# Kernel optimization log

Measured on AMD Instinct MI355X. Metric: run time of the kernel, lower is better.

Reference implementation:

```python
import jax, jax.numpy as jnp
import numpy as np

TOPK = 2
RENORMALIZE = True

T, H, I, E = 2048, 2048, 5632, 8  # tokens, hidden, intermediate, experts


def setup_inputs() -> dict:
    key = jax.random.key(0)
    k1, k2, k3, k4 = jax.random.split(key, 4)
    x = jax.random.normal(k1, (T, H), dtype=jnp.float32)
    gating_output = jax.random.normal(k2, (T, E), dtype=jnp.float32)
    # gate_up_proj: concat of gate [E,I,H] and up [E,I,H] along dim 1 -> [E,2I,H]
    w1 = jax.random.normal(k3, (E, 2 * I, H), dtype=jnp.float32) * 0.02
    # down_proj: [E, H, I]
    w2 = jax.random.normal(k4, (E, H, I), dtype=jnp.float32) * 0.02
    return {"x": x, "gating_output": gating_output, "w1": w1, "w2": w2}


def _route(gating_output):
    # standard (non-grouped) top-k softmax routing, renormalized
    probs = jax.nn.softmax(gating_output, axis=-1)            # [T, E]
    topk_w, topk_idx = jax.lax.top_k(probs, TOPK)             # [T, K]
    if RENORMALIZE:
        topk_w = topk_w / jnp.sum(topk_w, axis=-1, keepdims=True)
    t = gating_output.shape[0]
    route = jnp.zeros((t, gating_output.shape[1]), dtype=topk_w.dtype)
    route = route.at[jnp.arange(t)[:, None], topk_idx].set(topk_w)  # [T, E]
    return route


def reference(x, gating_output, w1, w2):
    route = _route(gating_output)                             # [T, E]
    inter = w2.shape[-1]
    out = jnp.zeros_like(x)
    # loop over small fixed expert count; each iter is dense GEMM work
    for e in range(w1.shape[0]):
        gu = x @ w1[e].T                                      # [T, 2I]
        h = jax.nn.silu(gu[:, :inter]) * gu[:, inter:]        # SwiGLU  [T, I]
        out = out + (h @ w2[e].T) * route[:, e:e + 1]         # [T, H]
    return out
```

## Files before the change

### kernel.cpp

```cpp
#include <hip/hip_runtime.h>
#include <hip/hip_bf16.h>


#define TT 2048
#define HH 2048
#define II 5632
#define NE 8

using f32x4  = __attribute__((ext_vector_type(4))) float;
using bf16x8 = __attribute__((ext_vector_type(8))) short;

__device__ __forceinline__ uint32_t bfbits(float f) {
    __hip_bfloat16 h = __float2bfloat16(f);
    unsigned short u;
    __builtin_memcpy(&u, &h, 2);
    return (uint32_t)u;
}
__device__ __forceinline__ uint32_t pk2(float a, float b) {
    return bfbits(a) | (bfbits(b) << 16);
}
__device__ __forceinline__ uint4 pk8(const float4& a, const float4& b) {
    uint4 r;
    r.x = pk2(a.x, a.y); r.y = pk2(a.z, a.w);
    r.z = pk2(b.x, b.y); r.w = pk2(b.z, b.w);
    return r;
}

__global__ void cvt_x(const float* __restrict__ x, __hip_bfloat16* __restrict__ xb) {
    const int i = (blockIdx.x * 256 + threadIdx.x) * 8;
    float4 a = *(const float4*)(x + i);
    float4 b = *(const float4*)(x + i + 4);
    *(uint4*)(xb + i) = pk8(a, b);
}

__global__ void route_topk(const float* __restrict__ gating,
                           int* __restrict__ tk_idx, float* __restrict__ tk_w) {
    int t = blockIdx.x * 256 + threadIdx.x;
    if (t >= TT) return;
    float g[NE];
#pragma unroll
    for (int e = 0; e < NE; e++) g[e] = gating[t * NE + e];
    int i0 = 0; float b0 = g[0];
#pragma unroll
    for (int e = 1; e < NE; e++) if (g[e] > b0) { b0 = g[e]; i0 = e; }
    int i1 = (i0 == 0) ? 1 : 0; float b1 = g[i1];
#pragma unroll
    for (int e = 0; e < NE; e++) if (e != i0 && g[e] > b1) { b1 = g[e]; i1 = e; }
    float ex = expf(b1 - b0);
    float w0 = 1.f / (1.f + ex);
    float w1 = ex / (1.f + ex);
    tk_idx[2 * t] = i0; tk_idx[2 * t + 1] = i1;
    tk_w[2 * t] = w0;  tk_w[2 * t + 1] = w1;
}

__global__ void build_lists(const int* __restrict__ tk_idx, const float* __restrict__ tk_w,
                            int* __restrict__ list_tok, float* __restrict__ list_w,
                            int* __restrict__ counts) {
    const int e = blockIdx.x;
    const int tid = threadIdx.x;
    int flag[8]; float wt[8];
    int cnt = 0;
#pragma unroll
    for (int j = 0; j < 8; j++) {
        int t = tid * 8 + j;
        int f = -1;
        if (tk_idx[2 * t] == e) f = 0;
        else if (tk_idx[2 * t + 1] == e) f = 1;
        flag[j] = f;
        wt[j] = (f >= 0) ? tk_w[2 * t + f] : 0.f;
        cnt += (f >= 0) ? 1 : 0;
    }
    __shared__ int s[256];
    s[tid] = cnt;
    __syncthreads();
    for (int d = 1; d < 256; d <<= 1) {
        int v = (tid >= d) ? s[tid - d] : 0;
        __syncthreads();
        s[tid] += v;
        __syncthreads();
    }
    int pos = s[tid] - cnt;
#pragma unroll
    for (int j = 0; j < 8; j++) {
        if (flag[j] >= 0) {
            list_tok[e * TT + pos] = tid * 8 + j;
            list_w[e * TT + pos] = wt[j];
            pos++;
        }
    }
    if (tid == 255) counts[e] = s[255];
}

__global__ __launch_bounds__(256, 2) void gemm1_swiglu(
    const __hip_bfloat16* __restrict__ xb, const float* __restrict__ w1,
    const int* __restrict__ list_tok, const int* __restrict__ counts,
    __hip_bfloat16* __restrict__ hbuf) {
    const int e = blockIdx.y >> 4;
    const int mt = blockIdx.y & 15;
    const int cnt = counts[e];
    const int row0 = mt * 128;
    if (row0 >= cnt) return;
    int off = 0;
#pragma unroll
    for (int i = 0; i < NE; i++) if (i < e) off += counts[i];
    const int valid = min(128, cnt - row0);
    const int n0 = blockIdx.x * 64;
    const int tid = threadIdx.x;

    __shared__ uint4 As[2][512];
    __shared__ uint4 Bg[2][256];
    __shared__ uint4 Bu[2][256];

    const int ar0 = tid >> 2, au = tid & 3;
    const int ar1 = ar0 + 64;
    const int tokA0 = list_tok[e * TT + row0 + min(ar0, valid - 1)];
    const int tokA1 = list_tok[e * TT + row0 + min(ar1, valid - 1)];
    const __hip_bfloat16* aS0 = xb + (size_t)tokA0 * HH + au * 8;
    const __hip_bfloat16* aS1 = xb + (size_t)tokA1 * HH + au * 8;
    const float* gS = w1 + (size_t)e * (2 * II) * HH + (size_t)(n0 + ar0) * HH + au * 8;
    const float* uS = gS + (size_t)II * HH;
    const int awi0 = ar0 * 4 + (au ^ ((ar0 >> 1) & 3));
    const int awi1 = ar1 * 4 + (au ^ ((ar1 >> 1) & 3));
    const int bwi  = ar0 * 4 + (au ^ ((ar0 >> 1) & 3));

    uint4 rA0, rA1; float4 rGa, rGb, rUa, rUb;
    auto LOAD = [&](int kt) {
        const int k = kt * 32;
        rGa  = *(const float4*)(gS + k);  rGb  = *(const float4*)(gS + k + 4);
        rUa  = *(const float4*)(uS + k);  rUb  = *(const float4*)(uS + k + 4);
        rA0  = *(const uint4*)(aS0 + k);
        rA1  = *(const uint4*)(aS1 + k);
    };
    auto STORE = [&](int b) {
        As[b][awi0] = rA0;
        As[b][awi1] = rA1;
        Bg[b][bwi]  = pk8(rGa, rGb);
        Bu[b][bwi]  = pk8(rUa, rUb);
    };

    const int lane = tid & 63;
    const int wv = tid >> 6;
    const int wm = wv >> 1, wn = wv & 1;
    const int l15 = lane & 15, ks = lane >> 4;
    int aidx[4], bidx[2];
#pragma unroll
    for (int m = 0; m < 4; m++) { int r = wm * 64 + m * 16 + l15; aidx[m] = r * 4 + (ks ^ ((r >> 1) & 3)); }
#pragma unroll
    for (int n = 0; n < 2; n++) { int c = wn * 32 + n * 16 + l15; bidx[n] = c * 4 + (ks ^ ((c >> 1) & 3)); }

    f32x4 accg[4][2], accu[4][2];
#pragma unroll
    for (int m = 0; m < 4; m++)
#pragma unroll
        for (int n = 0; n < 2; n++) { accg[m][n] = 0; accu[m][n] = 0; }

    LOAD(0); STORE(0); __syncthreads();
    const int KT = HH / 32;
#pragma unroll 2
    for (int kt = 0; kt < KT; ++kt) {
        const int cur = kt & 1;
        if (kt + 1 < KT) LOAD(kt + 1);
        bf16x8 af[4], gf[2], uf[2];
#pragma unroll
        for (int m = 0; m < 4; m++) { uint4 t = As[cur][aidx[m]]; af[m] = __builtin_bit_cast(bf16x8, t); }
#pragma unroll
        for (int n = 0; n < 2; n++) {
            uint4 t = Bg[cur][bidx[n]]; gf[n] = __builtin_bit_cast(bf16x8, t);
            uint4 t2 = Bu[cur][bidx[n]]; uf[n] = __builtin_bit_cast(bf16x8, t2);
        }
#pragma unroll
        for (int m = 0; m < 4; m++)
#pragma unroll
            for (int n = 0; n < 2; n++) {
                accg[m][n] = __builtin_amdgcn_mfma_f32_16x16x32_bf16(af[m], gf[n], accg[m][n], 0, 0, 0);
                accu[m][n] = __builtin_amdgcn_mfma_f32_16x16x32_bf16(af[m], uf[n], accu[m][n], 0, 0, 0);
            }
        if (kt + 1 < KT) STORE(cur ^ 1);
        __syncthreads();
    }

#pragma unroll
    for (int m = 0; m < 4; m++) {
#pragma unroll
        for (int r = 0; r < 4; r++) {
            const int lr = wm * 64 + m * 16 + ks * 4 + r;
            if (lr < valid) {
                __hip_bfloat16* hrow = hbuf + (size_t)(off + row0 + lr) * II;
#pragma unroll
                for (int n = 0; n < 2; n++) {
                    const int col = n0 + wn * 32 + n * 16 + l15;
                    float g = accg[m][n][r], u = accu[m][n][r];
                    float h = g / (1.f + __expf(-g)) * u;
                    hrow[col] = __float2bfloat16(h);
                }
            }
        }
    }
}

__global__ __launch_bounds__(256, 2) void gemm2_scatter(
    const __hip_bfloat16* __restrict__ hbuf, const float* __restrict__ w2,
    const int* __restrict__ list_tok, const float* __restrict__ list_w,
    const int* __restrict__ counts, float* __restrict__ out) {
    const int e = blockIdx.y >> 4;
    const int mt = blockIdx.y & 15;
    const int cnt = counts[e];
    const int row0 = mt * 128;
    if (row0 >= cnt) return;
    int off = 0;
#pragma unroll
    for (int i = 0; i < NE; i++) if (i < e) off += counts[i];
    const int valid = min(128, cnt - row0);
    const int n0 = blockIdx.x * 128;
    const int tid = threadIdx.x;

    __shared__ uint4 As[2][512];
    __shared__ uint4 Bs[2][512];

    const int ar0 = tid >> 2, au = tid & 3;
    const int ar1 = ar0 + 64;
    const size_t hr0 = (size_t)(off + row0 + min(ar0, valid - 1)) * II + au * 8;
    const size_t hr1 = (size_t)(off + row0 + min(ar1, valid - 1)) * II + au * 8;
    const float* bS0 = w2 + (size_t)e * HH * II + (size_t)(n0 + ar0) * II + au * 8;
    const float* bS1 = bS0 + (size_t)64 * II;
    const int awi0 = ar0 * 4 + (au ^ ((ar0 >> 1) & 3));
    const int awi1 = ar1 * 4 + (au ^ ((ar1 >> 1) & 3));

    uint4 rA0, rA1; float4 rB0a, rB0b, rB1a, rB1b;
    auto LOAD = [&](int kt) {
        const int k = kt * 32;
        rB0a = *(const float4*)(bS0 + k); rB0b = *(const float4*)(bS0 + k + 4);
        rB1a = *(const float4*)(bS1 + k); rB1b = *(const float4*)(bS1 + k + 4);
        rA0 = *(const uint4*)(hbuf + hr0 + k);
        rA1 = *(const uint4*)(hbuf + hr1 + k);
    };
    auto STORE = [&](int b) {
        As[b][awi0] = rA0;
        As[b][awi1] = rA1;
        Bs[b][awi0] = pk8(rB0a, rB0b);
        Bs[b][awi1] = pk8(rB1a, rB1b);
    };

    const int lane = tid & 63;
    const int wv = tid >> 6;
    const int wm = wv >> 1, wn = wv & 1;
    const int l15 = lane & 15, ks = lane >> 4;
    int aidx[4], bidx[4];
#pragma unroll
    for (int m = 0; m < 4; m++) { int r = wm * 64 + m * 16 + l15; aidx[m] = r * 4 + (ks ^ ((r >> 1) & 3)); }
#pragma unroll
    for (int n = 0; n < 4; n++) { int c = wn * 64 + n * 16 + l15; bidx[n] = c * 4 + (ks ^ ((c >> 1) & 3)); }

    f32x4 acc[4][4];
#pragma unroll
    for (int m = 0; m < 4; m++)
#pragma unroll
        for (int n = 0; n < 4; n++) acc[m][n] = 0;

    LOAD(0); STORE(0); __syncthreads();
    const int KT = II / 32;
#pragma unroll 2
    for (int kt = 0; kt < KT; ++kt) {
        const int cur = kt & 1;
        if (kt + 1 < KT) LOAD(kt + 1);
        bf16x8 af[4], bf[4];
#pragma unroll
        for (int m = 0; m < 4; m++) { uint4 t = As[cur][aidx[m]]; af[m] = __builtin_bit_cast(bf16x8, t); }
#pragma unroll
        for (int n = 0; n < 4; n++) { uint4 t = Bs[cur][bidx[n]]; bf[n] = __builtin_bit_cast(bf16x8, t); }
#pragma unroll
        for (int m = 0; m < 4; m++)
#pragma unroll
            for (int n = 0; n < 4; n++)
                acc[m][n] = __builtin_amdgcn_mfma_f32_16x16x32_bf16(af[m], bf[n], acc[m][n], 0, 0, 0);
        if (kt + 1 < KT) STORE(cur ^ 1);
        __syncthreads();
    }

#pragma unroll
    for (int m = 0; m < 4; m++) {
#pragma unroll
        for (int r = 0; r < 4; r++) {
            const int lr = wm * 64 + m * 16 + ks * 4 + r;
            if (lr < valid) {
                const int tok = list_tok[e * TT + row0 + lr];
                const float wt = list_w[e * TT + row0 + lr];
                float* orow = out + (size_t)tok * HH;
#pragma unroll
                for (int n = 0; n < 4; n++) {
                    const int col = n0 + wn * 64 + n * 16 + l15;
                    atomicAdd(orow + col, acc[m][n][r] * wt);
                }
            }
        }
    }
}

extern "C" void kernel_launch(void* const* d_in, const int* in_sizes, int n_in,
                              void* d_out, int out_size, void* d_ws, size_t ws_size,
                              hipStream_t stream) {
    const float* x      = (const float*)d_in[0];
    const float* gating = (const float*)d_in[1];
    const float* w1     = (const float*)d_in[2];
    const float* w2     = (const float*)d_in[3];
    float* out = (float*)d_out;
    char* ws = (char*)d_ws;

    int*   list_tok = (int*)(ws + 0);
    float* list_w   = (float*)(ws + (64 << 10));
    int*   counts   = (int*)(ws + (128 << 10));
    int*   tk_idx   = (int*)(ws + (132 << 10));
    float* tk_w     = (float*)(ws + (148 << 10));
    __hip_bfloat16* hbuf = (__hip_bfloat16*)(ws + (1 << 20));

    __hip_bfloat16* xb = (__hip_bfloat16*)d_out;

    route_topk<<<TT / 256, 256, 0, stream>>>(gating, tk_idx, tk_w);
    build_lists<<<NE, 256, 0, stream>>>(tk_idx, tk_w, list_tok, list_w, counts);
    cvt_x<<<TT * HH / (256 * 8), 256, 0, stream>>>(x, xb);
    gemm1_swiglu<<<dim3(II / 64, NE * 16), 256, 0, stream>>>(xb, w1, list_tok, counts, hbuf);
    (void)hipMemsetAsync(d_out, 0, (size_t)TT * HH * sizeof(float), stream);
    gemm2_scatter<<<dim3(HH / 128, NE * 16), 256, 0, stream>>>(hbuf, w2, list_tok, list_w, counts, out);
}
```

Baseline: 707.9 us.

## Use direct global-to-LDS loads with triple-buffered pipeline in both MoE GEMMs

Replaces the register-staged double-buffered loads in both expert GEMM kernels with global_load_lds transfers into a three-stage LDS ring, issuing loads three tiles ahead with explicit vmcnt waits. Weights are now kept as fp32 in LDS and converted to bf16 after the LDS read rather than before the store. This removes VGPR round-trips for staging and deepens latency hiding. In exchange it doubles LDS traffic and footprint for the weight tiles (fp32 instead of bf16), which may limit occupancy, and it adds an extra barrier per iteration.

```diff
diff --git a/kernel.cpp b/kernel.cpp
--- a/kernel.cpp
+++ b/kernel.cpp
@@ -25,6 +25,19 @@
     r.z = pk2(b.x, b.y); r.w = pk2(b.z, b.w);
     return r;
 }
+
+__device__ __forceinline__ void gl16(const void* g, void* l) {
+    __builtin_amdgcn_global_load_lds(
+        (const __attribute__((address_space(1))) unsigned int*)g,
+        (__attribute__((address_space(3))) unsigned int*)l, 16, 0, 0);
+}
+
+#define VMW(n) do { asm volatile("s_waitcnt vmcnt(" #n ")" ::: "memory"); \
+                    __builtin_amdgcn_sched_barrier(0); } while (0)
+#define LGKM0() do { asm volatile("s_waitcnt lgkmcnt(0)" ::: "memory"); \
+                     __builtin_amdgcn_sched_barrier(0); } while (0)
+#define BARR() do { __builtin_amdgcn_s_barrier(); \
+                    __builtin_amdgcn_sched_barrier(0); } while (0)
 
 __global__ void cvt_x(const float* __restrict__ x, __hip_bfloat16* __restrict__ xb) {
     const int i = (blockIdx.x * 256 + threadIdx.x) * 8;
@@ -106,47 +119,63 @@
     const int valid = min(128, cnt - row0);
     const int n0 = blockIdx.x * 64;
     const int tid = threadIdx.x;
-
-    __shared__ uint4 As[2][512];
-    __shared__ uint4 Bg[2][256];
-    __shared__ uint4 Bu[2][256];
-
-    const int ar0 = tid >> 2, au = tid & 3;
-    const int ar1 = ar0 + 64;
-    const int tokA0 = list_tok[e * TT + row0 + min(ar0, valid - 1)];
-    const int tokA1 = list_tok[e * TT + row0 + min(ar1, valid - 1)];
-    const __hip_bfloat16* aS0 = xb + (size_t)tokA0 * HH + au * 8;
-    const __hip_bfloat16* aS1 = xb + (size_t)tokA1 * HH + au * 8;
-    const float* gS = w1 + (size_t)e * (2 * II) * HH + (size_t)(n0 + ar0) * HH + au * 8;
-    const float* uS = gS + (size_t)II * HH;
-    const int awi0 = ar0 * 4 + (au ^ ((ar0 >> 1) & 3));
-    const int awi1 = ar1 * 4 + (au ^ ((ar1 >> 1) & 3));
-    const int bwi  = ar0 * 4 + (au ^ ((ar0 >> 1) & 3));
-
-    uint4 rA0, rA1; float4 rGa, rGb, rUa, rUb;
-    auto LOAD = [&](int kt) {
-        const int k = kt * 32;
-        rGa  = *(const float4*)(gS + k);  rGb  = *(const float4*)(gS + k + 4);
-        rUa  = *(const float4*)(uS + k);  rUb  = *(const float4*)(uS + k + 4);
-        rA0  = *(const uint4*)(aS0 + k);
-        rA1  = *(const uint4*)(aS1 + k);
+    const int w = tid >> 6, l = tid & 63;
+
+    __shared__ uint4  As[3 * 512];
+    __shared__ float4 Gs[3 * 512];
+    __shared__ float4 Us[3 * 512];
+
+    const char* aSrc0; const char* aSrc1;
+    {
+        int r0 = w * 16 + (l >> 2);
+        int r1 = 64 + r0;
+        int t0 = list_tok[e * TT + row0 + min(r0, valid - 1)];
+        int t1 = list_tok[e * TT + row0 + min(r1, valid - 1)];
+        int s0 = (l & 3) ^ ((r0 >> 1) & 3);
+        int s1 = (l & 3) ^ ((r1 >> 1) & 3);
+        aSrc0 = (const char*)(xb + (size_t)t0 * HH + s0 * 8);
+        aSrc1 = (const char*)(xb + (size_t)t1 * HH + s1 * 8);
+    }
+    const char *gSrc0, *gSrc1, *uSrc0, *uSrc1;
+    {
+        const float* base = w1 + (size_t)e * (2 * II) * HH;
+        int r0 = w * 8 + (l >> 3);
+        int r1 = 32 + r0;
+        int s0 = (l & 7) ^ (r0 & 7);
+        int s1 = (l & 7) ^ (r1 & 7);
+        gSrc0 = (const char*)(base + (size_t)(n0 + r0) * HH + s0 * 4);
+        gSrc1 = (const char*)(base + (size_t)(n0 + r1) * HH + s1 * 4);
+        uSrc0 = (const char*)(base + (size_t)(II + n0 + r0) * HH + s0 * 4);
+        uSrc1 = (const char*)(base + (size_t)(II + n0 + r1) * HH + s1 * 4);
+    }
+
+    auto STAGE = [&](int kt, int buf) {
+        const size_t kA = (size_t)kt * 64;
+        const size_t kB = (size_t)kt * 128;
+        char* ab = (char*)As + buf * 8192 + w * 1024;
+        gl16(aSrc0 + kA, ab);
+        gl16(aSrc1 + kA, ab + 4096);
+        char* gb = (char*)Gs + buf * 8192 + w * 1024;
+        gl16(gSrc0 + kB, gb);
+        gl16(gSrc1 + kB, gb + 4096);
+        char* ub = (char*)Us + buf * 8192 + w * 1024;
+        gl16(uSrc0 + kB, ub);
+        gl16(uSrc1 + kB, ub + 4096);
     };
-    auto STORE = [&](int b) {
-        As[b][awi0] = rA0;
-        As[b][awi1] = rA1;
-        Bg[b][bwi]  = pk8(rGa, rGb);
-        Bu[b][bwi]  = pk8(rUa, rUb);
-    };
-
-    const int lane = tid & 63;
-    const int wv = tid >> 6;
-    const int wm = wv >> 1, wn = wv & 1;
-    const int l15 = lane & 15, ks = lane >> 4;
-    int aidx[4], bidx[2];
+
+    const int wm = w >> 1, wn = w & 1;
+    const int l15 = l & 15, ks = l >> 4;
+    int aidx[4];
 #pragma unroll
     for (int m = 0; m < 4; m++) { int r = wm * 64 + m * 16 + l15; aidx[m] = r * 4 + (ks ^ ((r >> 1) & 3)); }
-#pragma unroll
-    for (int n = 0; n < 2; n++) { int c = wn * 32 + n * 16 + l15; bidx[n] = c * 4 + (ks ^ ((c >> 1) & 3)); }
+    int bbase[2], bo0[2], bo1[2];
+#pragma unroll
+    for (int n = 0; n < 2; n++) {
+        int c_ = wn * 32 + n * 16 + l15;
+        bbase[n] = c_ * 8;
+        bo0[n] = (2 * ks) ^ (c_ & 7);
+        bo1[n] = (2 * ks + 1) ^ (c_ & 7);
+    }
 
     f32x4 accg[4][2], accu[4][2];
 #pragma unroll
@@ -154,19 +183,37 @@
 #pragma unroll
         for (int n = 0; n < 2; n++) { accg[m][n] = 0; accu[m][n] = 0; }
 
-    LOAD(0); STORE(0); __syncthreads();
     const int KT = HH / 32;
-#pragma unroll 2
+    STAGE(0, 0); STAGE(1, 1); STAGE(2, 2);
+    VMW(12);
+    BARR();
+
+    int b = 0;
     for (int kt = 0; kt < KT; ++kt) {
-        const int cur = kt & 1;
-        if (kt + 1 < KT) LOAD(kt + 1);
-        bf16x8 af[4], gf[2], uf[2];
-#pragma unroll
-        for (int m = 0; m < 4; m++) { uint4 t = As[cur][aidx[m]]; af[m] = __builtin_bit_cast(bf16x8, t); }
+        bf16x8 af[4];
+        float4 glo[2], ghi[2], ulo[2], uhi[2];
+        {
+            const uint4*  Ab = As + b * 512;
+            const float4* Gb = Gs + b * 512;
+            const float4* Ub = Us + b * 512;
+#pragma unroll
+            for (int m = 0; m < 4; m++) { uint4 t = Ab[aidx[m]]; af[m] = __builtin_bit_cast(bf16x8, t); }
+#pragma unroll
+            for (int n = 0; n < 2; n++) {
+                glo[n] = Gb[bbase[n] + bo0[n]]; ghi[n] = Gb[bbase[n] + bo1[n]];
+                ulo[n] = Ub[bbase[n] + bo0[n]]; uhi[n] = Ub[bbase[n] + bo1[n]];
+            }
+        }
+        if (kt + 3 < KT) {
+            LGKM0();
+            BARR();
+            STAGE(kt + 3, b);
+        }
+        bf16x8 gf[2], uf[2];
 #pragma unroll
         for (int n = 0; n < 2; n++) {
-            uint4 t = Bg[cur][bidx[n]]; gf[n] = __builtin_bit_cast(bf16x8, t);
-            uint4 t2 = Bu[cur][bidx[n]]; uf[n] = __builtin_bit_cast(bf16x8, t2);
+            uint4 tg = pk8(glo[n], ghi[n]); gf[n] = __builtin_bit_cast(bf16x8, tg);
+            uint4 tu = pk8(ulo[n], uhi[n]); uf[n] = __builtin_bit_cast(bf16x8, tu);
         }
 #pragma unroll
         for (int m = 0; m < 4; m++)
@@ -175,8 +222,11 @@
                 accg[m][n] = __builtin_amdgcn_mfma_f32_16x16x32_bf16(af[m], gf[n], accg[m][n], 0, 0, 0);
                 accu[m][n] = __builtin_amdgcn_mfma_f32_16x16x32_bf16(af[m], uf[n], accu[m][n], 0, 0, 0);
             }
-        if (kt + 1 < KT) STORE(cur ^ 1);
-        __syncthreads();
+        if (kt + 3 < KT)      VMW(12);
+        else if (kt + 2 < KT) VMW(6);
+        else if (kt + 1 < KT) VMW(0);
+        if (kt + 1 < KT) BARR();
+        b = (b == 2) ? 0 : b + 1;
     }
 
 #pragma unroll
@@ -213,43 +263,59 @@
     const int valid = min(128, cnt - row0);
     const int n0 = blockIdx.x * 128;
     const int tid = threadIdx.x;
-
-    __shared__ uint4 As[2][512];
-    __shared__ uint4 Bs[2][512];
-
-    const int ar0 = tid >> 2, au = tid & 3;
-    const int ar1 = ar0 + 64;
-    const size_t hr0 = (size_t)(off + row0 + min(ar0, valid - 1)) * II + au * 8;
-    const size_t hr1 = (size_t)(off + row0 + min(ar1, valid - 1)) * II + au * 8;
-    const float* bS0 = w2 + (size_t)e * HH * II + (size_t)(n0 + ar0) * II + au * 8;
-    const float* bS1 = bS0 + (size_t)64 * II;
-    const int awi0 = ar0 * 4 + (au ^ ((ar0 >> 1) & 3));
-    const int awi1 = ar1 * 4 + (au ^ ((ar1 >> 1) & 3));
-
-    uint4 rA0, rA1; float4 rB0a, rB0b, rB1a, rB1b;
-    auto LOAD = [&](int kt) {
-        const int k = kt * 32;
-        rB0a = *(const float4*)(bS0 + k); rB0b = *(const float4*)(bS0 + k + 4);
-        rB1a = *(const float4*)(bS1 + k); rB1b = *(const float4*)(bS1 + k + 4);
-        rA0 = *(const uint4*)(hbuf + hr0 + k);
-        rA1 = *(const uint4*)(hbuf + hr1 + k);
+    const int w = tid >> 6, l = tid & 63;
+
+    __shared__ uint4  As[3 * 512];
+    __shared__ float4 Bs[3 * 1024];
+
+    const char* aSrc0; const char* aSrc1;
+    {
+        int r0 = w * 16 + (l >> 2);
+        int r1 = 64 + r0;
+        int s0 = (l & 3) ^ ((r0 >> 1) & 3);
+        int s1 = (l & 3) ^ ((r1 >> 1) & 3);
+        size_t h0 = (size_t)(off + row0 + min(r0, valid - 1)) * II;
+        size_t h1 = (size_t)(off + row0 + min(r1, valid - 1)) * II;
+        aSrc0 = (const char*)(hbuf + h0 + s0 * 8);
+        aSrc1 = (const char*)(hbuf + h1 + s1 * 8);
+    }
+    const char* bSrc[4];
+    {
+        const float* base = w2 + (size_t)e * HH * II;
+#pragma unroll
+        for (int c = 0; c < 4; c++) {
+            int r = c * 32 + w * 8 + (l >> 3);
+            int s = (l & 7) ^ (r & 7);
+            bSrc[c] = (const char*)(base + (size_t)(n0 + r) * II + s * 4);
+        }
+    }
+
+    auto STAGE = [&](int kt, int buf) {
+        const size_t kA = (size_t)kt * 64;
+        const size_t kB = (size_t)kt * 128;
+        char* ab = (char*)As + buf * 8192 + w * 1024;
+        gl16(aSrc0 + kA, ab);
+        gl16(aSrc1 + kA, ab + 4096);
+        char* bb = (char*)Bs + buf * 16384 + w * 1024;
+        gl16(bSrc[0] + kB, bb);
+        gl16(bSrc[1] + kB, bb + 4096);
+        gl16(bSrc[2] + kB, bb + 8192);
+        gl16(bSrc[3] + kB, bb + 12288);
     };
-    auto STORE = [&](int b) {
-        As[b][awi0] = rA0;
-        As[b][awi1] = rA1;
-        Bs[b][awi0] = pk8(rB0a, rB0b);
-        Bs[b][awi1] = pk8(rB1a, rB1b);
-    };
-
-    const int lane = tid & 63;
-    const int wv = tid >> 6;
-    const int wm = wv >> 1, wn = wv & 1;
-    const int l15 = lane & 15, ks = lane >> 4;
-    int aidx[4], bidx[4];
+
+    const int wm = w >> 1, wn = w & 1;
+    const int l15 = l & 15, ks = l >> 4;
+    int aidx[4];
 #pragma unroll
     for (int m = 0; m < 4; m++) { int r = wm * 64 + m * 16 + l15; aidx[m] = r * 4 + (ks ^ ((r >> 1) & 3)); }
-#pragma unroll
-    for (int n = 0; n < 4; n++) { int c = wn * 64 + n * 16 + l15; bidx[n] = c * 4 + (ks ^ ((c >> 1) & 3)); }
+    int bbase[4], bo0[4], bo1[4];
+#pragma unroll
+    for (int n = 0; n < 4; n++) {
+        int c_ = wn * 64 + n * 16 + l15;
+        bbase[n] = c_ * 8;
+        bo0[n] = (2 * ks) ^ (c_ & 7);
+        bo1[n] = (2 * ks + 1) ^ (c_ & 7);
+    }
 
     f32x4 acc[4][4];
 #pragma unroll
@@ -257,24 +323,46 @@
 #pragma unroll
         for (int n = 0; n < 4; n++) acc[m][n] = 0;
 
-    LOAD(0); STORE(0); __syncthreads();
     const int KT = II / 32;
-#pragma unroll 2
+    STAGE(0, 0); STAGE(1, 1); STAGE(2, 2);
+    VMW(12);
+    BARR();
+
+    int b = 0;
     for (int kt = 0; kt < KT; ++kt) {
-        const int cur = kt & 1;
-        if (kt + 1 < KT) LOAD(kt + 1);
-        bf16x8 af[4], bf[4];
-#pragma unroll
-        for (int m = 0; m < 4; m++) { uint4 t = As[cur][aidx[m]]; af[m] = __builtin_bit_cast(bf16x8, t); }
-#pragma unroll
-        for (int n = 0; n < 4; n++) { uint4 t = Bs[cur][bidx[n]]; bf[n] = __builtin_bit_cast(bf16x8, t); }
+        bf16x8 af[4];
+        float4 blo[4], bhi[4];
+        {
+            const uint4*  Ab = As + b * 512;
+            const float4* Bb = Bs + b * 1024;
+#pragma unroll
+            for (int m = 0; m < 4; m++) { uint4 t = Ab[aidx[m]]; af[m] = __builtin_bit_cast(bf16x8, t); }
+#pragma unroll
+            for (int n = 0; n < 4; n++) {
+                blo[n] = Bb[bbase[n] + bo0[n]];
+                bhi[n] = Bb[bbase[n] + bo1[n]];
+            }
+        }
+        if (kt + 3 < KT) {
+            LGKM0();
+            BARR();
+            STAGE(kt + 3, b);
+        }
+        bf16x8 bf[4];
+#pragma unroll
+        for (int n = 0; n < 4; n++) {
+            uint4 t = pk8(blo[n], bhi[n]); bf[n] = __builtin_bit_cast(bf16x8, t);
+        }
 #pragma unroll
         for (int m = 0; m < 4; m++)
 #pragma unroll
             for (int n = 0; n < 4; n++)
                 acc[m][n] = __builtin_amdgcn_mfma_f32_16x16x32_bf16(af[m], bf[n], acc[m][n], 0, 0, 0);
-        if (kt + 1 < KT) STORE(cur ^ 1);
-        __syncthreads();
+        if (kt + 3 < KT)      VMW(12);
+        else if (kt + 2 < KT) VMW(6);
+        else if (kt + 1 < KT) VMW(0);
+        if (kt + 1 < KT) BARR();
+        b = (b == 2) ? 0 : b + 1;
     }
 
 #pragma unroll
```

New measurement: 790.6 us. +11.7%, slower.

## Load A-operand fragments directly from global into registers, bypassing LDS

Applied to the files above, without the earlier changes.

Both MoE GEMM kernels now have each lane read its MFMA A-fragments (gathered token rows of x, or rows of hbuf) straight from global memory into registers, double-buffered across k-steps. The A shared-memory tiles and their stores and reads are removed. This cuts LDS traffic and footprint, which may allow more resident blocks. In exchange, A rows are fetched redundantly by the two N-waves that share them, and the 16-byte per-lane loads are strided across rows, so global and L2 traffic for A rises.

```diff
diff --git a/kernel.cpp b/kernel.cpp
--- a/kernel.cpp
+++ b/kernel.cpp
@@ -107,44 +107,38 @@
     const int n0 = blockIdx.x * 64;
     const int tid = threadIdx.x;
 
-    __shared__ uint4 As[2][512];
     __shared__ uint4 Bg[2][256];
     __shared__ uint4 Bu[2][256];
 
     const int ar0 = tid >> 2, au = tid & 3;
-    const int ar1 = ar0 + 64;
-    const int tokA0 = list_tok[e * TT + row0 + min(ar0, valid - 1)];
-    const int tokA1 = list_tok[e * TT + row0 + min(ar1, valid - 1)];
-    const __hip_bfloat16* aS0 = xb + (size_t)tokA0 * HH + au * 8;
-    const __hip_bfloat16* aS1 = xb + (size_t)tokA1 * HH + au * 8;
     const float* gS = w1 + (size_t)e * (2 * II) * HH + (size_t)(n0 + ar0) * HH + au * 8;
     const float* uS = gS + (size_t)II * HH;
-    const int awi0 = ar0 * 4 + (au ^ ((ar0 >> 1) & 3));
-    const int awi1 = ar1 * 4 + (au ^ ((ar1 >> 1) & 3));
-    const int bwi  = ar0 * 4 + (au ^ ((ar0 >> 1) & 3));
-
-    uint4 rA0, rA1; float4 rGa, rGb, rUa, rUb;
-    auto LOAD = [&](int kt) {
+    const int bwi = ar0 * 4 + (au ^ ((ar0 >> 1) & 3));
+
+    float4 rGa, rGb, rUa, rUb;
+    auto LOADB = [&](int kt) {
         const int k = kt * 32;
-        rGa  = *(const float4*)(gS + k);  rGb  = *(const float4*)(gS + k + 4);
-        rUa  = *(const float4*)(uS + k);  rUb  = *(const float4*)(uS + k + 4);
-        rA0  = *(const uint4*)(aS0 + k);
-        rA1  = *(const uint4*)(aS1 + k);
+        rGa = *(const float4*)(gS + k); rGb = *(const float4*)(gS + k + 4);
+        rUa = *(const float4*)(uS + k); rUb = *(const float4*)(uS + k + 4);
     };
-    auto STORE = [&](int b) {
-        As[b][awi0] = rA0;
-        As[b][awi1] = rA1;
-        Bg[b][bwi]  = pk8(rGa, rGb);
-        Bu[b][bwi]  = pk8(rUa, rUb);
+    auto STOREB = [&](int b) {
+        Bg[b][bwi] = pk8(rGa, rGb);
+        Bu[b][bwi] = pk8(rUa, rUb);
     };
 
     const int lane = tid & 63;
     const int wv = tid >> 6;
     const int wm = wv >> 1, wn = wv & 1;
     const int l15 = lane & 15, ks = lane >> 4;
-    int aidx[4], bidx[2];
-#pragma unroll
-    for (int m = 0; m < 4; m++) { int r = wm * 64 + m * 16 + l15; aidx[m] = r * 4 + (ks ^ ((r >> 1) & 3)); }
+
+    const __hip_bfloat16* aP[4];
+#pragma unroll
+    for (int m = 0; m < 4; m++) {
+        int r = wm * 64 + m * 16 + l15;
+        int tok = list_tok[e * TT + row0 + min(r, valid - 1)];
+        aP[m] = xb + (size_t)tok * HH + ks * 8;
+    }
+    int bidx[2];
 #pragma unroll
     for (int n = 0; n < 2; n++) { int c = wn * 32 + n * 16 + l15; bidx[n] = c * 4 + (ks ^ ((c >> 1) & 3)); }
 
@@ -154,28 +148,41 @@
 #pragma unroll
         for (int n = 0; n < 2; n++) { accg[m][n] = 0; accu[m][n] = 0; }
 
-    LOAD(0); STORE(0); __syncthreads();
+    uint4 aC[4], aN[4];
+#pragma unroll
+    for (int m = 0; m < 4; m++) aC[m] = *(const uint4*)(aP[m]);
+    LOADB(0); STOREB(0);
+    __syncthreads();
+
     const int KT = HH / 32;
 #pragma unroll 2
     for (int kt = 0; kt < KT; ++kt) {
         const int cur = kt & 1;
-        if (kt + 1 < KT) LOAD(kt + 1);
-        bf16x8 af[4], gf[2], uf[2];
-#pragma unroll
-        for (int m = 0; m < 4; m++) { uint4 t = As[cur][aidx[m]]; af[m] = __builtin_bit_cast(bf16x8, t); }
+        if (kt + 1 < KT) {
+            LOADB(kt + 1);
+#pragma unroll
+            for (int m = 0; m < 4; m++) aN[m] = *(const uint4*)(aP[m] + (kt + 1) * 32);
+        }
+        bf16x8 gf[2], uf[2];
 #pragma unroll
         for (int n = 0; n < 2; n++) {
             uint4 t = Bg[cur][bidx[n]]; gf[n] = __builtin_bit_cast(bf16x8, t);
             uint4 t2 = Bu[cur][bidx[n]]; uf[n] = __builtin_bit_cast(bf16x8, t2);
         }
 #pragma unroll
-        for (int m = 0; m < 4; m++)
+        for (int m = 0; m < 4; m++) {
+            bf16x8 af = __builtin_bit_cast(bf16x8, aC[m]);
 #pragma unroll
             for (int n = 0; n < 2; n++) {
-                accg[m][n] = __builtin_amdgcn_mfma_f32_16x16x32_bf16(af[m], gf[n], accg[m][n], 0, 0, 0);
-                accu[m][n] = __builtin_amdgcn_mfma_f32_16x16x32_bf16(af[m], uf[n], accu[m][n], 0, 0, 0);
+                accg[m][n] = __builtin_amdgcn_mfma_f32_16x16x32_bf16(af, gf[n], accg[m][n], 0, 0, 0);
+                accu[m][n] = __builtin_amdgcn_mfma_f32_16x16x32_bf16(af, uf[n], accu[m][n], 0, 0, 0);
             }
-        if (kt + 1 < KT) STORE(cur ^ 1);
+        }
+        if (kt + 1 < KT) {
+            STOREB(cur ^ 1);
+#pragma unroll
+            for (int m = 0; m < 4; m++) aC[m] = aN[m];
+        }
         __syncthreads();
     }
 
@@ -214,40 +221,38 @@
     const int n0 = blockIdx.x * 128;
     const int tid = threadIdx.x;
 
-    __shared__ uint4 As[2][512];
     __shared__ uint4 Bs[2][512];
 
     const int ar0 = tid >> 2, au = tid & 3;
     const int ar1 = ar0 + 64;
-    const size_t hr0 = (size_t)(off + row0 + min(ar0, valid - 1)) * II + au * 8;
-    const size_t hr1 = (size_t)(off + row0 + min(ar1, valid - 1)) * II + au * 8;
     const float* bS0 = w2 + (size_t)e * HH * II + (size_t)(n0 + ar0) * II + au * 8;
     const float* bS1 = bS0 + (size_t)64 * II;
-    const int awi0 = ar0 * 4 + (au ^ ((ar0 >> 1) & 3));
-    const int awi1 = ar1 * 4 + (au ^ ((ar1 >> 1) & 3));
-
-    uint4 rA0, rA1; float4 rB0a, rB0b, rB1a, rB1b;
-    auto LOAD = [&](int kt) {
+    const int bwi0 = ar0 * 4 + (au ^ ((ar0 >> 1) & 3));
+    const int bwi1 = ar1 * 4 + (au ^ ((ar1 >> 1) & 3));
+
+    float4 rB0a, rB0b, rB1a, rB1b;
+    auto LOADB = [&](int kt) {
         const int k = kt * 32;
         rB0a = *(const float4*)(bS0 + k); rB0b = *(const float4*)(bS0 + k + 4);
         rB1a = *(const float4*)(bS1 + k); rB1b = *(const float4*)(bS1 + k + 4);
-        rA0 = *(const uint4*)(hbuf + hr0 + k);
-        rA1 = *(const uint4*)(hbuf + hr1 + k);
     };
-    auto STORE = [&](int b) {
-        As[b][awi0] = rA0;
-        As[b][awi1] = rA1;
-        Bs[b][awi0] = pk8(rB0a, rB0b);
-        Bs[b][awi1] = pk8(rB1a, rB1b);
+    auto STOREB = [&](int b) {
+        Bs[b][bwi0] = pk8(rB0a, rB0b);
+        Bs[b][bwi1] = pk8(rB1a, rB1b);
     };
 
     const int lane = tid & 63;
     const int wv = tid >> 6;
     const int wm = wv >> 1, wn = wv & 1;
     const int l15 = lane & 15, ks = lane >> 4;
-    int aidx[4], bidx[4];
-#pragma unroll
-    for (int m = 0; m < 4; m++) { int r = wm * 64 + m * 16 + l15; aidx[m] = r * 4 + (ks ^ ((r >> 1) & 3)); }
+
+    const __hip_bfloat16* aP[4];
+#pragma unroll
+    for (int m = 0; m < 4; m++) {
+        int r = wm * 64 + m * 16 + l15;
+        aP[m] = hbuf + (size_t)(off + row0 + min(r, valid - 1)) * II + ks * 8;
+    }
+    int bidx[4];
 #pragma unroll
     for (int n = 0; n < 4; n++) { int c = wn * 64 + n * 16 + l15; bidx[n] = c * 4 + (ks ^ ((c >> 1) & 3)); }
 
@@ -257,23 +262,36 @@
 #pragma unroll
         for (int n = 0; n < 4; n++) acc[m][n] = 0;
 
-    LOAD(0); STORE(0); __syncthreads();
+    uint4 aC[4], aN[4];
+#pragma unroll
+    for (int m = 0; m < 4; m++) aC[m] = *(const uint4*)(aP[m]);
+    LOADB(0); STOREB(0);
+    __syncthreads();
+
     const int KT = II / 32;
 #pragma unroll 2
     for (int kt = 0; kt < KT; ++kt) {
         const int cur = kt & 1;
-        if (kt + 1 < KT) LOAD(kt + 1);
-        bf16x8 af[4], bf[4];
-#pragma unroll
-        for (int m = 0; m < 4; m++) { uint4 t = As[cur][aidx[m]]; af[m] = __builtin_bit_cast(bf16x8, t); }
+        if (kt + 1 < KT) {
+            LOADB(kt + 1);
+#pragma unroll
+            for (int m = 0; m < 4; m++) aN[m] = *(const uint4*)(aP[m] + (kt + 1) * 32);
+        }
+        bf16x8 bf[4];
 #pragma unroll
         for (int n = 0; n < 4; n++) { uint4 t = Bs[cur][bidx[n]]; bf[n] = __builtin_bit_cast(bf16x8, t); }
 #pragma unroll
-        for (int m = 0; m < 4; m++)
+        for (int m = 0; m < 4; m++) {
+            bf16x8 af = __builtin_bit_cast(bf16x8, aC[m]);
 #pragma unroll
             for (int n = 0; n < 4; n++)
-                acc[m][n] = __builtin_amdgcn_mfma_f32_16x16x32_bf16(af[m], bf[n], acc[m][n], 0, 0, 0);
-        if (kt + 1 < KT) STORE(cur ^ 1);
+                acc[m][n] = __builtin_amdgcn_mfma_f32_16x16x32_bf16(af, bf[n], acc[m][n], 0, 0, 0);
+        }
+        if (kt + 1 < KT) {
+            STOREB(cur ^ 1);
+#pragma unroll
+            for (int m = 0; m < 4; m++) aC[m] = aN[m];
+        }
         __syncthreads();
     }
 
```

Result: slower. 940.3 us (+32.8%).
